# Performance work log

Measured on AMD Instinct MI355X. Metric: run time of the kernel, lower is better.

## Reference

```python
import jax, jax.numpy as jnp
import numpy as np

N, E, C, K = 50000, 800000, 64, 8
D = C * K  # 512
NEG_SLOPE = 0.01  # torch leaky_relu default


def setup_inputs() -> dict:
    key = jax.random.key(0)
    ks = jax.random.split(key, 6)
    x = jax.random.normal(ks[0], (N, D), dtype=jnp.float32)
    edge_index = jax.random.randint(ks[1], (2, E), 0, N, dtype=jnp.int64)
    conv_W = jax.random.normal(ks[2], (K, C, C), dtype=jnp.float32) * (1.0 / np.sqrt(C))
    conv_b = jax.random.normal(ks[3], (K, C), dtype=jnp.float32) * 0.01
    W1 = jax.random.normal(ks[4], (D, D), dtype=jnp.float32) * (1.0 / np.sqrt(D))
    W2 = jax.random.normal(ks[5], (D, D), dtype=jnp.float32) * (1.0 / np.sqrt(D))
    return {"x": x, "edge_index": edge_index, "conv_W": conv_W,
            "conv_b": conv_b, "W1": W1, "W2": W2}


def _gcn_conv(xk, Wk, bk, src, dst, dinv, n):
    # PyG GCNConv: transform, then symmetric-normalized aggregation with self-loops,
    # then add bias.
    xt = xk @ Wk.T  # [N, C]
    norm = dinv[src] * dinv[dst]  # [E]
    agg = jax.ops.segment_sum(norm[:, None] * xt[src], dst, num_segments=n)
    agg = agg + (dinv * dinv)[:, None] * xt  # self-loop contribution
    return agg + bk


def reference(x, edge_index, conv_W, conv_b, W1, W2):
    n = x.shape[0]
    src, dst = edge_index[0], edge_index[1]
    # degree with self-loops (edge weight 1)
    deg = jax.ops.segment_sum(jnp.ones((E,), x.dtype), dst, num_segments=n) + 1.0
    dinv = deg ** -0.5
    xr = x.reshape(n, C, K)
    zs = [jax.nn.leaky_relu(_gcn_conv(xr[:, :, i], conv_W[i], conv_b[i], src, dst, dinv, n),
                            negative_slope=NEG_SLOPE)
          for i in range(K)]
    z = jnp.concatenate(zs, axis=1)  # [N, D]
    z = jax.nn.leaky_relu(z, negative_slope=NEG_SLOPE)
    # dropout is identity in eval mode (dr=12 is invalid for torch Dropout anyway)
    z_fc1 = z @ W1.T
    z_fc2 = z @ W2.T
    s = jnp.sum(z_fc1.T @ z_fc2, axis=0)  # [D]
    # softmax over axis 0 of a [1, D] tensor (as in the original code)
    gate = jax.nn.softmax((s / jnp.sqrt(jnp.asarray(D, x.dtype)))[None, :], axis=0)
    return z * gate
```

## Files before the change

### kernel.cpp

```cpp
#include <hip/hip_runtime.h>

#define NN 50000
#define EE 800000
#define KK 8
#define DD 512
#define CAP 64

typedef __attribute__((ext_vector_type(8))) short short8;
typedef __attribute__((ext_vector_type(4))) float f32x4;

__device__ __forceinline__ float leaky2(float v) {
    v = (v < 0.0f) ? 0.01f * v : v;
    v = (v < 0.0f) ? 0.01f * v : v;
    return v;
}

__device__ __forceinline__ unsigned short f2bf(float f) {
    unsigned u = __float_as_uint(f);
    u += 0x7fffu + ((u >> 16) & 1u);
    return (unsigned short)(u >> 16);
}
__device__ __forceinline__ float bf_lo(unsigned u) { return __uint_as_float(u << 16); }
__device__ __forceinline__ float bf_hi(unsigned u) { return __uint_as_float(u & 0xffff0000u); }

__device__ __forceinline__ void fma8(float acc[8], float w, uint4 v) {
    acc[0] += w * bf_lo(v.x); acc[1] += w * bf_hi(v.x);
    acc[2] += w * bf_lo(v.y); acc[3] += w * bf_hi(v.y);
    acc[4] += w * bf_lo(v.z); acc[5] += w * bf_hi(v.z);
    acc[6] += w * bf_lo(v.w); acc[7] += w * bf_hi(v.w);
}

__global__ void k_zero(int* __restrict__ cursor) {
    int i = blockIdx.x * 256 + threadIdx.x;
    if (i < NN) cursor[i] = 0;
}

__global__ void k_wconv(const float* __restrict__ W, unsigned short* __restrict__ Wbf) {
    int i = blockIdx.x * 256 + threadIdx.x;
    if (i < KK * 64 * 64) Wbf[i] = f2bf(W[i]);
}

__global__ void k_fill(const int* __restrict__ ei, int* __restrict__ cursor,
                       int* __restrict__ bw) {
    int e = blockIdx.x * 256 + threadIdx.x;
    if (e < EE) {
        int s = ei[e];
        int d = ei[EE + e];
        int p = atomicAdd(&cursor[d], 1);
        if (p < CAP) bw[(size_t)d * CAP + p] = s;
    }
}

__global__ void k_dinv(const int* __restrict__ cursor, float* __restrict__ dinv) {
    int i = blockIdx.x * 256 + threadIdx.x;
    if (i < NN) dinv[i] = rsqrtf((float)cursor[i] + 1.0f);
}

__global__ __launch_bounds__(256) void k_transform(const float* __restrict__ x,
                                                   const unsigned short* __restrict__ Wbf,
                                                   unsigned short* __restrict__ xt) {
    __shared__ unsigned short lxT[32 * 8 * 64];
    const int t = threadIdx.x;
    const int n0 = blockIdx.x * 32;

    const float4* x4 = (const float4*)x;
    #pragma unroll
    for (int i = 0; i < 16; i++) {
        int idx = i * 256 + t;
        int n = idx >> 7;
        int q = idx & 127;
        int n_eff = n0 + n; if (n_eff >= NN) n_eff = NN - 1;
        float4 v = x4[(size_t)n_eff * 128 + q];
        int c = q >> 1;
        int k0 = (q & 1) * 4;
        unsigned short* p = &lxT[(n * 8 + k0) * 64 + c];
        p[0] = f2bf(v.x); p[64] = f2bf(v.y); p[128] = f2bf(v.z); p[192] = f2bf(v.w);
    }
    __syncthreads();

    const int wv   = t >> 6;
    const int lane = t & 63;
    const int l15  = lane & 15;
    const int quad = lane >> 4;
    const f32x4 zero = {0.f, 0.f, 0.f, 0.f};

    #pragma unroll
    for (int kk = 0; kk < 2; kk++) {
        const int k = wv * 2 + kk;
        short8 afr[4][2];
        #pragma unroll
        for (int jt = 0; jt < 4; jt++)
            #pragma unroll
            for (int ks = 0; ks < 2; ks++)
                afr[jt][ks] = *(const short8*)&Wbf[k * 4096 + (jt * 16 + l15) * 64 + ks * 32 + quad * 8];

        #pragma unroll
        for (int ng = 0; ng < 2; ng++) {
            short8 bfr[2];
            #pragma unroll
            for (int ks = 0; ks < 2; ks++)
                bfr[ks] = *(const short8*)&lxT[((ng * 16 + l15) * 8 + k) * 64 + ks * 32 + quad * 8];
            f32x4 acc[4];
            #pragma unroll
            for (int jt = 0; jt < 4; jt++) {
                acc[jt] = zero;
                acc[jt] = __builtin_amdgcn_mfma_f32_16x16x32_bf16(afr[jt][0], bfr[0], acc[jt], 0, 0, 0);
                acc[jt] = __builtin_amdgcn_mfma_f32_16x16x32_bf16(afr[jt][1], bfr[1], acc[jt], 0, 0, 0);
            }
            const int node = n0 + ng * 16 + l15;
            if (node < NN) {
                #pragma unroll
                for (int jt = 0; jt < 4; jt++) {
                    ushort4 h;
                    h.x = f2bf(acc[jt][0]); h.y = f2bf(acc[jt][1]);
                    h.z = f2bf(acc[jt][2]); h.w = f2bf(acc[jt][3]);
                    *(ushort4*)&xt[(size_t)node * DD + k * 64 + jt * 16 + quad * 4] = h;
                }
            }
        }
    }
}

__global__ __launch_bounds__(256) void k_agg(const unsigned short* __restrict__ xt,
                                             const float* __restrict__ dinv,
                                             const int* __restrict__ cursor,
                                             const int* __restrict__ bw,
                                             const float* __restrict__ bias,
                                             float* __restrict__ out) {
    const int n = __builtin_amdgcn_readfirstlane(blockIdx.x * 4 + (threadIdx.x >> 6));
    const int lane = threadIdx.x & 63;
    const float dn = dinv[n];
    int cn = cursor[n]; if (cn > CAP) cn = CAP;

    const uint4* xt4 = (const uint4*)xt;
    uint4 a = xt4[(size_t)n * 64 + lane];
    const float sw = dn * dn;
    float acc[8];
    acc[0] = bf_lo(a.x) * sw; acc[1] = bf_hi(a.x) * sw;
    acc[2] = bf_lo(a.y) * sw; acc[3] = bf_hi(a.y) * sw;
    acc[4] = bf_lo(a.z) * sw; acc[5] = bf_hi(a.z) * sw;
    acc[6] = bf_lo(a.w) * sw; acc[7] = bf_hi(a.w) * sw;

    const int* bk = bw + (size_t)n * CAP;
    int i = 0;
    if (cn >= 2) {
        int sa = bk[0], sb = bk[1];
        uint4 va = xt4[(size_t)sa * 64 + lane];
        uint4 vb = xt4[(size_t)sb * 64 + lane];
        float wa = dn * dinv[sa], wb = dn * dinv[sb];
        for (i = 2; i + 1 < cn; i += 2) {
            int sc = bk[i], sd = bk[i + 1];
            uint4 vc = xt4[(size_t)sc * 64 + lane];
            uint4 vd = xt4[(size_t)sd * 64 + lane];
            float wc = dn * dinv[sc], wd = dn * dinv[sd];
            fma8(acc, wa, va); fma8(acc, wb, vb);
            wa = wc; wb = wd; va = vc; vb = vd;
        }
        fma8(acc, wa, va); fma8(acc, wb, vb);
    }
    for (; i < cn; ++i) {
        int s = bk[i];
        uint4 v = xt4[(size_t)s * 64 + lane];
        float w = dn * dinv[s];
        fma8(acc, w, v);
    }

    const float4* b4 = (const float4*)bias;
    float4 b0 = b4[lane * 2], b1 = b4[lane * 2 + 1];
    f32x4 r0, r1;
    r0[0] = leaky2(acc[0] + b0.x); r0[1] = leaky2(acc[1] + b0.y);
    r0[2] = leaky2(acc[2] + b0.z); r0[3] = leaky2(acc[3] + b0.w);
    r1[0] = leaky2(acc[4] + b1.x); r1[1] = leaky2(acc[5] + b1.y);
    r1[2] = leaky2(acc[6] + b1.z); r1[3] = leaky2(acc[7] + b1.w);
    f32x4* o4 = (f32x4*)(out + (size_t)n * DD);
    __builtin_nontemporal_store(r0, o4 + lane * 2);
    __builtin_nontemporal_store(r1, o4 + lane * 2 + 1);
}

extern "C" void kernel_launch(void* const* d_in, const int* in_sizes, int n_in,
                              void* d_out, int out_size, void* d_ws, size_t ws_size,
                              hipStream_t stream) {
    const float* x  = (const float*)d_in[0];
    const int*   ei = (const int*)d_in[1];
    const float* W  = (const float*)d_in[2];
    const float* b  = (const float*)d_in[3];
    float* out = (float*)d_out;

    unsigned short* xt = (unsigned short*)d_ws;
    float* dinv   = (float*)(xt + (size_t)NN * DD);
    int*   cursor = (int*)(dinv + NN);
    int*   bw     = cursor + NN;
    unsigned short* wbf = (unsigned short*)(bw + (size_t)NN * CAP);

    k_zero <<<(NN + 255) / 256, 256, 0, stream>>>(cursor);
    k_wconv<<<(KK * 64 * 64 + 255) / 256, 256, 0, stream>>>(W, wbf);
    k_fill <<<(EE + 255) / 256, 256, 0, stream>>>(ei, cursor, bw);
    k_dinv <<<(NN + 255) / 256, 256, 0, stream>>>(cursor, dinv);
    k_transform<<<(NN + 31) / 32, 256, 0, stream>>>(x, wbf, xt);
    k_agg<<<NN / 4, 256, 0, stream>>>(xt, dinv, cursor, bw, b, out);
}
```

Before: 382.0 us.

## Fold source dinv into transform output and load neighbor list via lane broadcast

Pre-scales each transformed row by its own dinv in the transform kernel, so aggregation becomes a plain sum scaled by the destination dinv at the end. This removes the per-edge dinv gather and multiply. The neighbor index list is now loaded once per wave as one coalesced read and broadcast with readlane, replacing scalar loads per edge, and a sched_barrier pins load/compute ordering. Rounding the pre-scaled value to bf16 changes numerics slightly. Reading bw by lane may touch uninitialized slots beyond the node's degree, but those values are never used.

Measured after the change: 380.3 us. About the same (-0.4%).

```diff
diff --git a/kernel.cpp b/kernel.cpp
--- a/kernel.cpp
+++ b/kernel.cpp
@@ -23,11 +23,11 @@
 __device__ __forceinline__ float bf_lo(unsigned u) { return __uint_as_float(u << 16); }
 __device__ __forceinline__ float bf_hi(unsigned u) { return __uint_as_float(u & 0xffff0000u); }
 
-__device__ __forceinline__ void fma8(float acc[8], float w, uint4 v) {
-    acc[0] += w * bf_lo(v.x); acc[1] += w * bf_hi(v.x);
-    acc[2] += w * bf_lo(v.y); acc[3] += w * bf_hi(v.y);
-    acc[4] += w * bf_lo(v.z); acc[5] += w * bf_hi(v.z);
-    acc[6] += w * bf_lo(v.w); acc[7] += w * bf_hi(v.w);
+__device__ __forceinline__ void add8(float acc[8], uint4 v) {
+    acc[0] += bf_lo(v.x); acc[1] += bf_hi(v.x);
+    acc[2] += bf_lo(v.y); acc[3] += bf_hi(v.y);
+    acc[4] += bf_lo(v.z); acc[5] += bf_hi(v.z);
+    acc[6] += bf_lo(v.w); acc[7] += bf_hi(v.w);
 }
 
 __global__ void k_zero(int* __restrict__ cursor) {
@@ -58,6 +58,7 @@
 
 __global__ __launch_bounds__(256) void k_transform(const float* __restrict__ x,
                                                    const unsigned short* __restrict__ Wbf,
+                                                   const float* __restrict__ dinv,
                                                    unsigned short* __restrict__ xt) {
     __shared__ unsigned short lxT[32 * 8 * 64];
     const int t = threadIdx.x;
@@ -109,11 +110,12 @@
             }
             const int node = n0 + ng * 16 + l15;
             if (node < NN) {
+                const float dv = dinv[node];
                 #pragma unroll
                 for (int jt = 0; jt < 4; jt++) {
                     ushort4 h;
-                    h.x = f2bf(acc[jt][0]); h.y = f2bf(acc[jt][1]);
-                    h.z = f2bf(acc[jt][2]); h.w = f2bf(acc[jt][3]);
+                    h.x = f2bf(acc[jt][0] * dv); h.y = f2bf(acc[jt][1] * dv);
+                    h.z = f2bf(acc[jt][2] * dv); h.w = f2bf(acc[jt][3] * dv);
                     *(ushort4*)&xt[(size_t)node * DD + k * 64 + jt * 16 + quad * 4] = h;
                 }
             }
@@ -133,45 +135,45 @@
     int cn = cursor[n]; if (cn > CAP) cn = CAP;
 
     const uint4* xt4 = (const uint4*)xt;
+    int bidx = bw[(size_t)n * CAP + lane];
     uint4 a = xt4[(size_t)n * 64 + lane];
-    const float sw = dn * dn;
+
     float acc[8];
-    acc[0] = bf_lo(a.x) * sw; acc[1] = bf_hi(a.x) * sw;
-    acc[2] = bf_lo(a.y) * sw; acc[3] = bf_hi(a.y) * sw;
-    acc[4] = bf_lo(a.z) * sw; acc[5] = bf_hi(a.z) * sw;
-    acc[6] = bf_lo(a.w) * sw; acc[7] = bf_hi(a.w) * sw;
-
-    const int* bk = bw + (size_t)n * CAP;
+    acc[0] = bf_lo(a.x); acc[1] = bf_hi(a.x);
+    acc[2] = bf_lo(a.y); acc[3] = bf_hi(a.y);
+    acc[4] = bf_lo(a.z); acc[5] = bf_hi(a.z);
+    acc[6] = bf_lo(a.w); acc[7] = bf_hi(a.w);
+
     int i = 0;
     if (cn >= 2) {
-        int sa = bk[0], sb = bk[1];
+        int sa = __builtin_amdgcn_readlane(bidx, 0);
+        int sb = __builtin_amdgcn_readlane(bidx, 1);
         uint4 va = xt4[(size_t)sa * 64 + lane];
         uint4 vb = xt4[(size_t)sb * 64 + lane];
-        float wa = dn * dinv[sa], wb = dn * dinv[sb];
         for (i = 2; i + 1 < cn; i += 2) {
-            int sc = bk[i], sd = bk[i + 1];
+            int sc = __builtin_amdgcn_readlane(bidx, i);
+            int sd = __builtin_amdgcn_readlane(bidx, i + 1);
             uint4 vc = xt4[(size_t)sc * 64 + lane];
             uint4 vd = xt4[(size_t)sd * 64 + lane];
-            float wc = dn * dinv[sc], wd = dn * dinv[sd];
-            fma8(acc, wa, va); fma8(acc, wb, vb);
-            wa = wc; wb = wd; va = vc; vb = vd;
+            __builtin_amdgcn_sched_barrier(0);
+            add8(acc, va); add8(acc, vb);
+            va = vc; vb = vd;
         }
-        fma8(acc, wa, va); fma8(acc, wb, vb);
+        add8(acc, va); add8(acc, vb);
     }
     for (; i < cn; ++i) {
-        int s = bk[i];
+        int s = __builtin_amdgcn_readlane(bidx, i);
         uint4 v = xt4[(size_t)s * 64 + lane];
-        float w = dn * dinv[s];
-        fma8(acc, w, v);
+        add8(acc, v);
     }
 
     const float4* b4 = (const float4*)bias;
     float4 b0 = b4[lane * 2], b1 = b4[lane * 2 + 1];
     f32x4 r0, r1;
-    r0[0] = leaky2(acc[0] + b0.x); r0[1] = leaky2(acc[1] + b0.y);
-    r0[2] = leaky2(acc[2] + b0.z); r0[3] = leaky2(acc[3] + b0.w);
-    r1[0] = leaky2(acc[4] + b1.x); r1[1] = leaky2(acc[5] + b1.y);
-    r1[2] = leaky2(acc[6] + b1.z); r1[3] = leaky2(acc[7] + b1.w);
+    r0[0] = leaky2(dn * acc[0] + b0.x); r0[1] = leaky2(dn * acc[1] + b0.y);
+    r0[2] = leaky2(dn * acc[2] + b0.z); r0[3] = leaky2(dn * acc[3] + b0.w);
+    r1[0] = leaky2(dn * acc[4] + b1.x); r1[1] = leaky2(dn * acc[5] + b1.y);
+    r1[2] = leaky2(dn * acc[6] + b1.z); r1[3] = leaky2(dn * acc[7] + b1.w);
     f32x4* o4 = (f32x4*)(out + (size_t)n * DD);
     __builtin_nontemporal_store(r0, o4 + lane * 2);
     __builtin_nontemporal_store(r1, o4 + lane * 2 + 1);
@@ -196,6 +198,6 @@
     k_wconv<<<(KK * 64 * 64 + 255) / 256, 256, 0, stream>>>(W, wbf);
     k_fill <<<(EE + 255) / 256, 256, 0, stream>>>(ei, cursor, bw);
     k_dinv <<<(NN + 255) / 256, 256, 0, stream>>>(cursor, dinv);
-    k_transform<<<(NN + 31) / 32, 256, 0, stream>>>(x, wbf, xt);
+    k_transform<<<(NN + 31) / 32, 256, 0, stream>>>(x, wbf, dinv, xt);
     k_agg<<<NN / 4, 256, 0, stream>>>(xt, dinv, cursor, bw, b, out);
 }
```
